# Kernel optimization log

Hardware: AMD Instinct MI355X
Metric: run time of the kernel (lower is better)

## Reference

```python
import jax, jax.numpy as jnp
import numpy as np

B, N, E = 16, 50000, 1600000  # batch, num_nodes (excl. ground), num_edges


def setup_inputs() -> dict:
    key = jax.random.key(0)
    k1, k2, k3, k4 = jax.random.split(key, 4)
    x = jax.random.normal(k1, (B, N), dtype=jnp.float32)
    # node indices in [0, N]; index 0 is the ground node prepended in forward
    src_node = jax.random.randint(k2, (E,), 0, N + 1)
    des_node = jax.random.randint(k3, (E,), 0, N + 1)
    # per-edge device params (a, w, b), gauss init std=0.01 per _init_model_param
    param = jax.random.normal(k4, (3, E), dtype=jnp.float32) * 0.01
    t = jnp.zeros((1,), dtype=jnp.float32)
    return {"t": t, "x": x, "param": param, "src_node": src_node, "des_node": des_node}


def _edge_model(param, v_s, v_d):
    # per-edge nonlinear device current: i_e = a_e * tanh(w_e*(v_s - v_d) + b_e)
    a, w, b = param[0], param[1], param[2]
    return a * jnp.tanh(w * (v_s - v_d) + b)  # (B, E)


def reference(t, x, param, src_node, des_node):
    # prepend ground node (voltage 0) -> aux_v: (B, N+1)
    aux_v = jnp.concatenate([jnp.zeros_like(x[..., :1]), x], axis=-1)
    v_s = aux_v[:, src_node]  # gather (B, E)
    v_d = aux_v[:, des_node]  # gather (B, E)
    state_i = _edge_model(param, v_s, v_d)  # (B, E)
    # KCL: current leaves src, enters des; scatter_add along node axis
    res = jnp.zeros_like(aux_v)
    res = res.at[:, src_node].add(-state_i)
    res = res.at[:, des_node].add(state_i)
    return res[:, 1:]  # drop ground node
```

## Files before the change

### kernel.cpp

```cpp
#include <hip/hip_runtime.h>

#define BATCH 16
#define PS 49
#define NPART 1024
#define SB 256
#define TPB 1024
#define LDSCAP 3840

#define TWO_LOG2E 2.8853900817779268f

__global__ __launch_bounds__(TPB)
void hist1(const int* __restrict__ src, const int* __restrict__ des,
           const float* __restrict__ x, float* __restrict__ auxT,
           unsigned* __restrict__ blockHist, int E, int n) {
    __shared__ unsigned h[NPART];
    __shared__ float tile[64 * 17];
    int tid = threadIdx.x;
    for (int i = tid; i < NPART; i += TPB) h[i] = 0;
    if (blockIdx.x == 0 && tid < BATCH) auxT[tid] = 0.0f;
    int nTiles = (n + 63) / 64;
    for (int t0 = blockIdx.x; t0 < nTiles; t0 += gridDim.x) {
        int i0 = t0 * 64;
        int b = tid >> 6, ii = tid & 63;
        float v = (i0 + ii < n) ? x[(size_t)b * n + i0 + ii] : 0.0f;
        __syncthreads();
        tile[ii * 17 + b] = v;
        __syncthreads();
        int i2 = i0 + (tid >> 4);
        if (i2 < n)
            auxT[(size_t)(i2 + 1) * BATCH + (tid & 15)] = tile[(tid >> 4) * 17 + (tid & 15)];
    }
    __syncthreads();
    long t = (long)blockIdx.x * TPB + tid;
    long stride = (long)gridDim.x * TPB * 4;
    for (long e0 = t * 4; e0 < E; e0 += stride) {
        int ne = (int)min((long)4, (long)E - e0);
        int ss[4], dd[4];
        if (ne == 4) {
            int4 sv = *(const int4*)(src + e0);
            int4 dv = *(const int4*)(des + e0);
            ss[0]=sv.x; ss[1]=sv.y; ss[2]=sv.z; ss[3]=sv.w;
            dd[0]=dv.x; dd[1]=dv.y; dd[2]=dv.z; dd[3]=dv.w;
        } else {
            for (int j = 0; j < ne; ++j) { ss[j] = src[e0+j]; dd[j] = des[e0+j]; }
        }
        for (int j = 0; j < ne; ++j) {
            atomicAdd(&h[ss[j] / PS], 1u);
            atomicAdd(&h[dd[j] / PS], 1u);
        }
    }
    __syncthreads();
    for (int i = tid; i < NPART; i += TPB)
        blockHist[(size_t)blockIdx.x * NPART + i] = h[i];
}

__global__ __launch_bounds__(TPB)
void totals_k(const unsigned* __restrict__ blockHist, unsigned* __restrict__ binTotal) {
    int tid = threadIdx.x;
    int bin = blockIdx.x * 64 + (tid >> 4);
    int j = tid & 15;
    unsigned s = 0;
    for (int r = j; r < SB; r += 16) s += blockHist[(size_t)r * NPART + bin];
#pragma unroll
    for (int m = 1; m < 16; m <<= 1) s += __shfl_xor(s, m, 64);
    if (j == 0) binTotal[bin] = s;
}

__global__ __launch_bounds__(TPB)
void scan_bins(const unsigned* __restrict__ binTotal, unsigned* __restrict__ partStart) {
    __shared__ unsigned wsum[16];
    int tid = threadIdx.x;
    int lane = tid & 63, wv = tid >> 6;
    unsigned v = binTotal[tid];
    unsigned inc = v;
    for (int off = 1; off < 64; off <<= 1) {
        unsigned t = __shfl_up(inc, off, 64);
        if (lane >= off) inc += t;
    }
    if (lane == 63) wsum[wv] = inc;
    __syncthreads();
    if (tid < 16) {
        unsigned w = wsum[tid], winc = w;
        for (int off = 1; off < 16; off <<= 1) {
            unsigned t = __shfl_up(winc, off, 64);
            if (tid >= off) winc += t;
        }
        wsum[tid] = winc - w;
    }
    __syncthreads();
    unsigned excl = (inc - v) + wsum[wv];
    partStart[tid] = excl;
    if (tid == TPB - 1) partStart[NPART] = excl + v;
}

__global__ __launch_bounds__(TPB)
void offs_k(unsigned* __restrict__ blockHist, const unsigned* __restrict__ partStart) {
    int tid = threadIdx.x;
    int binLocal = tid >> 4;
    int bin = blockIdx.x * 64 + binLocal;
    int j = tid & 15;
    const int per = SB / 16;
    unsigned ls = 0;
    for (int r = j * per; r < (j + 1) * per; ++r)
        ls += blockHist[(size_t)r * NPART + bin];
    int waveBase = (binLocal & 3) * 16;
    unsigned excl = 0;
    for (int k = 0; k < 16; ++k) {
        unsigned v = __shfl(ls, waveBase + k, 64);
        if (k < j) excl += v;
    }
    unsigned run = partStart[bin] + excl;
    for (int r = j * per; r < (j + 1) * per; ++r) {
        unsigned tmp = blockHist[(size_t)r * NPART + bin];
        blockHist[(size_t)r * NPART + bin] = run;
        run += tmp;
    }
}

__global__ __launch_bounds__(TPB)
void scatter1(const int* __restrict__ src, const int* __restrict__ des,
              const float* __restrict__ param, const unsigned* __restrict__ offsets,
              uint4* __restrict__ bins, int E) {
    __shared__ unsigned offs[NPART];
    int tid = threadIdx.x;
    for (int i = tid; i < NPART; i += TPB)
        offs[i] = offsets[(size_t)blockIdx.x * NPART + i];
    __syncthreads();
    long t = (long)blockIdx.x * TPB + tid;
    long stride = (long)gridDim.x * TPB * 4;
    for (long e0 = t * 4; e0 < E; e0 += stride) {
        int ne = (int)min((long)4, (long)E - e0);
        int ss[4], dd[4];
        float aa[4], ww[4], cc[4];
        if (ne == 4) {
            int4 sv = *(const int4*)(src + e0);
            int4 dv = *(const int4*)(des + e0);
            float4 av = *(const float4*)(param + e0);
            float4 wv = *(const float4*)(param + E + e0);
            float4 cv = *(const float4*)(param + 2 * (size_t)E + e0);
            ss[0]=sv.x; ss[1]=sv.y; ss[2]=sv.z; ss[3]=sv.w;
            dd[0]=dv.x; dd[1]=dv.y; dd[2]=dv.z; dd[3]=dv.w;
            aa[0]=av.x; aa[1]=av.y; aa[2]=av.z; aa[3]=av.w;
            ww[0]=wv.x; ww[1]=wv.y; ww[2]=wv.z; ww[3]=wv.w;
            cc[0]=cv.x; cc[1]=cv.y; cc[2]=cv.z; cc[3]=cv.w;
        } else {
            for (int j = 0; j < ne; ++j) {
                ss[j] = src[e0+j]; dd[j] = des[e0+j];
                aa[j] = param[e0+j]; ww[j] = param[E + e0 + j];
                cc[j] = param[2 * (size_t)E + e0 + j];
            }
        }
        for (int j = 0; j < ne; ++j) {
            int s = ss[j], d = dd[j];
            float wq = ww[j] * TWO_LOG2E, cq = cc[j] * TWO_LOG2E;
            unsigned slot = atomicAdd(&offs[s / PS], 1u);
            bins[slot] = make_uint4((unsigned)s | ((unsigned)d << 16),
                                    __float_as_uint(-aa[j]), __float_as_uint(wq),
                                    __float_as_uint(cq));
            unsigned slot2 = atomicAdd(&offs[d / PS], 1u);
            bins[slot2] = make_uint4((unsigned)d | ((unsigned)s << 16),
                                     __float_as_uint(aa[j]), __float_as_uint(-wq),
                                     __float_as_uint(cq));
        }
    }
}

static __device__ __forceinline__ float edge_eval(float a, float a2, float wq, float cq,
                                                  float dv) {
    float ez = __builtin_amdgcn_exp2f(__builtin_fmaf(wq, dv, cq));
    float r = __builtin_amdgcn_rcpf(ez + 1.0f);
    return __builtin_fmaf(-a2, r, a);
}

__global__ __launch_bounds__(TPB)
void sort_accumulate(const uint4* __restrict__ bins, const unsigned* __restrict__ partStart,
                     const float* __restrict__ auxT, float* __restrict__ out, int n) {
    extern __shared__ uint4 srec[];
    unsigned* bump = (unsigned*)(srec + LDSCAP);
    unsigned* ns   = bump + PS;
    int p = blockIdx.x;
    int tid = threadIdx.x;
    int lane = tid & 63;
    int wv = tid >> 6;
    unsigned lo = partStart[p], hi = partStart[p + 1];
    unsigned cl = min(hi - lo, (unsigned)LDSCAP);
    int base = p * PS;

    for (int i = tid; i < PS; i += TPB) bump[i] = 0;
    __syncthreads();
    const unsigned* keys = (const unsigned*)bins;
    for (unsigned k = tid; k < cl; k += TPB) {
        unsigned o = keys[(size_t)(lo + k) * 4] & 0xFFFFu;
        atomicAdd(&bump[o - (unsigned)base], 1u);
    }
    __syncthreads();
    if (wv == 0) {
        unsigned v = (lane < PS) ? bump[lane] : 0u;
        unsigned inc = v;
        for (int off = 1; off < 64; off <<= 1) {
            unsigned t = __shfl_up(inc, off, 64);
            if (lane >= off) inc += t;
        }
        unsigned excl = inc - v;
        if (lane < PS) { ns[lane] = excl; bump[lane] = excl; }
        if (lane == PS - 1) ns[PS] = inc;
    }
    __syncthreads();
    for (unsigned k = tid; k < cl; k += TPB) {
        uint4 rec = bins[lo + k];
        unsigned slot = atomicAdd(&bump[(rec.x & 0xFFFFu) - (unsigned)base], 1u);
        srec[slot] = rec;
    }
    __syncthreads();
    int ri = lane >> 2, lj = lane & 3;
    const float4* aux4 = (const float4*)auxT;
    for (int nl = wv; nl < PS; nl += TPB / 64) {
        int node = base + nl;
        if (node == 0 || node > n) continue;
        unsigned l2 = ns[nl], h2 = ns[nl + 1];
        float4 vo = aux4[(size_t)node * 4 + lj];
        float ax = 0.0f, ay = 0.0f, az = 0.0f, as_ = 0.0f;
        for (unsigned kk = l2; kk < h2; kk += 16) {
            unsigned k = kk + (unsigned)ri;
            uint4 rec;
            if (k < h2) rec = srec[k];
            else { rec.x = 0u; rec.y = 0u; rec.z = 0u; rec.w = 0u; }
            unsigned rem = rec.x >> 16;
            float4 vr = aux4[(size_t)rem * 4 + lj];
            float a = __uint_as_float(rec.y);
            float a2 = a + a;
            float wq = __uint_as_float(rec.z);
            float cq = __uint_as_float(rec.w);
            ax  += edge_eval(a, a2, wq, cq, vo.x - vr.x);
            ay  += edge_eval(a, a2, wq, cq, vo.y - vr.y);
            az  += edge_eval(a, a2, wq, cq, vo.z - vr.z);
            as_ += edge_eval(a, a2, wq, cq, vo.w - vr.w);
        }
        for (unsigned kk = lo + cl; kk < hi; kk += 16) {
            unsigned k = kk + (unsigned)ri;
            uint4 rec;
            if (k < hi) rec = bins[k];
            else { rec.x = 0u; rec.y = 0u; rec.z = 0u; rec.w = 0u; }
            if ((int)(rec.x & 0xFFFFu) != node) rec.y = 0u;
            unsigned rem = rec.x >> 16;
            float4 vr = aux4[(size_t)rem * 4 + lj];
            float a = __uint_as_float(rec.y);
            float a2 = a + a;
            float wq = __uint_as_float(rec.z);
            float cq = __uint_as_float(rec.w);
            ax  += edge_eval(a, a2, wq, cq, vo.x - vr.x);
            ay  += edge_eval(a, a2, wq, cq, vo.y - vr.y);
            az  += edge_eval(a, a2, wq, cq, vo.z - vr.z);
            as_ += edge_eval(a, a2, wq, cq, vo.w - vr.w);
        }
#pragma unroll
        for (int m = 4; m < 64; m <<= 1) {
            ax  += __shfl_xor(ax, m, 64);
            ay  += __shfl_xor(ay, m, 64);
            az  += __shfl_xor(az, m, 64);
            as_ += __shfl_xor(as_, m, 64);
        }
        if (lane < 4) {
            int j = node - 1;
            int b0 = lj * 4;
            out[(size_t)(b0 + 0) * n + j] = ax;
            out[(size_t)(b0 + 1) * n + j] = ay;
            out[(size_t)(b0 + 2) * n + j] = az;
            out[(size_t)(b0 + 3) * n + j] = as_;
        }
    }
}

__global__ void edge_direct(const float* __restrict__ param,
                            const int* __restrict__ src,
                            const int* __restrict__ des,
                            const float* __restrict__ x,
                            float* __restrict__ out, int E, int n) {
    int e = blockIdx.x * blockDim.x + threadIdx.x;
    if (e >= E) return;
    float a = param[e], w = param[E + e], c = param[2 * E + e];
    int s = src[e], d = des[e];
#pragma unroll
    for (int b = 0; b < BATCH; ++b) {
        float vs = s ? x[(size_t)b * n + (s - 1)] : 0.0f;
        float vd = d ? x[(size_t)b * n + (d - 1)] : 0.0f;
        float st = a * tanhf(w * (vs - vd) + c);
        if (s) atomicAdd(out + (size_t)b * n + (s - 1), -st);
        if (d) atomicAdd(out + (size_t)b * n + (d - 1), st);
    }
}

extern "C" void kernel_launch(void* const* d_in, const int* in_sizes, int n_in,
                              void* d_out, int out_size, void* d_ws, size_t ws_size,
                              hipStream_t stream) {
    const float* x     = (const float*)d_in[1];
    const float* param = (const float*)d_in[2];
    const int*   src   = (const int*)d_in[3];
    const int*   des   = (const int*)d_in[4];
    float* out = (float*)d_out;

    int E = in_sizes[3];
    int n = in_sizes[1] / BATCH;

    auto alignup = [](size_t v) { return (v + 255) & ~(size_t)255; };
    size_t auxBytes  = alignup((size_t)(n + 1) * BATCH * sizeof(float));
    size_t bhBytes   = alignup((size_t)SB * NPART * sizeof(unsigned));
    size_t psBytes   = alignup((size_t)(NPART + 1) * sizeof(unsigned));
    size_t btBytes   = alignup((size_t)NPART * sizeof(unsigned));
    size_t binBytes  = alignup((size_t)2 * E * sizeof(uint4));
    size_t need      = auxBytes + bhBytes + psBytes + btBytes + binBytes;

    size_t saLds = (size_t)LDSCAP * sizeof(uint4) + (2 * PS + 1 + 8) * sizeof(unsigned);

    if (ws_size >= need && (n + 1) <= NPART * PS && n <= 65534) {
        char* w = (char*)d_ws;
        float*    auxT      = (float*)w;     w += auxBytes;
        unsigned* blockHist = (unsigned*)w;  w += bhBytes;
        unsigned* partStart = (unsigned*)w;  w += psBytes;
        unsigned* binTotal  = (unsigned*)w;  w += btBytes;
        uint4*    bins      = (uint4*)w;

        hist1<<<SB, TPB, 0, stream>>>(src, des, x, auxT, blockHist, E, n);
        totals_k<<<NPART / 64, TPB, 0, stream>>>(blockHist, binTotal);
        scan_bins<<<1, TPB, 0, stream>>>(binTotal, partStart);
        offs_k<<<NPART / 64, TPB, 0, stream>>>(blockHist, partStart);
        scatter1<<<SB, TPB, 0, stream>>>(src, des, param, blockHist, bins, E);
        sort_accumulate<<<NPART, TPB, saLds, stream>>>(bins, partStart, auxT, out, n);
        return;
    }

    (void)hipMemsetAsync(out, 0, (size_t)out_size * sizeof(float), stream);
    edge_direct<<<(E + 255) / 256, 256, 0, stream>>>(param, src, des, x, out, E, n);
}
```

Baseline: 114.0 us.

## Split scatter into two bin-half passes and reuse atomic ranks in local sort

The scatter kernel now makes two passes over the edges, each covering half of the partitions with a half-size shared offset table. The intent is to narrow the write footprint per pass and cut the shared-memory needed per block, at the cost of reading the edge arrays twice. In the per-partition sort, the rank returned by the counting atomic is kept in registers and reused for placement, which removes the second atomic pass. The sort relies on at most four records per thread (4*TPB = 4096 ≥ LDSCAP = 3840).

```diff
diff --git a/kernel.cpp b/kernel.cpp
--- a/kernel.cpp
+++ b/kernel.cpp
@@ -121,46 +121,55 @@
 void scatter1(const int* __restrict__ src, const int* __restrict__ des,
               const float* __restrict__ param, const unsigned* __restrict__ offsets,
               uint4* __restrict__ bins, int E) {
-    __shared__ unsigned offs[NPART];
-    int tid = threadIdx.x;
-    for (int i = tid; i < NPART; i += TPB)
-        offs[i] = offsets[(size_t)blockIdx.x * NPART + i];
-    __syncthreads();
-    long t = (long)blockIdx.x * TPB + tid;
-    long stride = (long)gridDim.x * TPB * 4;
-    for (long e0 = t * 4; e0 < E; e0 += stride) {
-        int ne = (int)min((long)4, (long)E - e0);
-        int ss[4], dd[4];
-        float aa[4], ww[4], cc[4];
-        if (ne == 4) {
-            int4 sv = *(const int4*)(src + e0);
-            int4 dv = *(const int4*)(des + e0);
-            float4 av = *(const float4*)(param + e0);
-            float4 wv = *(const float4*)(param + E + e0);
-            float4 cv = *(const float4*)(param + 2 * (size_t)E + e0);
-            ss[0]=sv.x; ss[1]=sv.y; ss[2]=sv.z; ss[3]=sv.w;
-            dd[0]=dv.x; dd[1]=dv.y; dd[2]=dv.z; dd[3]=dv.w;
-            aa[0]=av.x; aa[1]=av.y; aa[2]=av.z; aa[3]=av.w;
-            ww[0]=wv.x; ww[1]=wv.y; ww[2]=wv.z; ww[3]=wv.w;
-            cc[0]=cv.x; cc[1]=cv.y; cc[2]=cv.z; cc[3]=cv.w;
-        } else {
+    __shared__ unsigned offs[NPART / 2];
+    int tid = threadIdx.x;
+    for (int half = 0; half < 2; ++half) {
+        int binLo = half * (NPART / 2);
+        __syncthreads();
+        for (int i = tid; i < NPART / 2; i += TPB)
+            offs[i] = offsets[(size_t)blockIdx.x * NPART + binLo + i];
+        __syncthreads();
+        long t = (long)blockIdx.x * TPB + tid;
+        long stride = (long)gridDim.x * TPB * 4;
+        for (long e0 = t * 4; e0 < E; e0 += stride) {
+            int ne = (int)min((long)4, (long)E - e0);
+            int ss[4], dd[4];
+            float aa[4], ww[4], cc[4];
+            if (ne == 4) {
+                int4 sv = *(const int4*)(src + e0);
+                int4 dv = *(const int4*)(des + e0);
+                float4 av = *(const float4*)(param + e0);
+                float4 wv = *(const float4*)(param + E + e0);
+                float4 cv = *(const float4*)(param + 2 * (size_t)E + e0);
+                ss[0]=sv.x; ss[1]=sv.y; ss[2]=sv.z; ss[3]=sv.w;
+                dd[0]=dv.x; dd[1]=dv.y; dd[2]=dv.z; dd[3]=dv.w;
+                aa[0]=av.x; aa[1]=av.y; aa[2]=av.z; aa[3]=av.w;
+                ww[0]=wv.x; ww[1]=wv.y; ww[2]=wv.z; ww[3]=wv.w;
+                cc[0]=cv.x; cc[1]=cv.y; cc[2]=cv.z; cc[3]=cv.w;
+            } else {
+                for (int j = 0; j < ne; ++j) {
+                    ss[j] = src[e0+j]; dd[j] = des[e0+j];
+                    aa[j] = param[e0+j]; ww[j] = param[E + e0 + j];
+                    cc[j] = param[2 * (size_t)E + e0 + j];
+                }
+            }
             for (int j = 0; j < ne; ++j) {
-                ss[j] = src[e0+j]; dd[j] = des[e0+j];
-                aa[j] = param[e0+j]; ww[j] = param[E + e0 + j];
-                cc[j] = param[2 * (size_t)E + e0 + j];
+                int s = ss[j], d = dd[j];
+                float wq = ww[j] * TWO_LOG2E, cq = cc[j] * TWO_LOG2E;
+                int ps = s / PS, pd = d / PS;
+                if ((ps >> 9) == half) {
+                    unsigned slot = atomicAdd(&offs[ps & 511], 1u);
+                    bins[slot] = make_uint4((unsigned)s | ((unsigned)d << 16),
+                                            __float_as_uint(-aa[j]), __float_as_uint(wq),
+                                            __float_as_uint(cq));
+                }
+                if ((pd >> 9) == half) {
+                    unsigned slot2 = atomicAdd(&offs[pd & 511], 1u);
+                    bins[slot2] = make_uint4((unsigned)d | ((unsigned)s << 16),
+                                             __float_as_uint(aa[j]), __float_as_uint(-wq),
+                                             __float_as_uint(cq));
+                }
             }
-        }
-        for (int j = 0; j < ne; ++j) {
-            int s = ss[j], d = dd[j];
-            float wq = ww[j] * TWO_LOG2E, cq = cc[j] * TWO_LOG2E;
-            unsigned slot = atomicAdd(&offs[s / PS], 1u);
-            bins[slot] = make_uint4((unsigned)s | ((unsigned)d << 16),
-                                    __float_as_uint(-aa[j]), __float_as_uint(wq),
-                                    __float_as_uint(cq));
-            unsigned slot2 = atomicAdd(&offs[d / PS], 1u);
-            bins[slot2] = make_uint4((unsigned)d | ((unsigned)s << 16),
-                                     __float_as_uint(aa[j]), __float_as_uint(-wq),
-                                     __float_as_uint(cq));
         }
     }
 }
@@ -189,10 +198,17 @@
     for (int i = tid; i < PS; i += TPB) bump[i] = 0;
     __syncthreads();
     const unsigned* keys = (const unsigned*)bins;
-    for (unsigned k = tid; k < cl; k += TPB) {
-        unsigned o = keys[(size_t)(lo + k) * 4] & 0xFFFFu;
-        atomicAdd(&bump[o - (unsigned)base], 1u);
-    }
+    unsigned o0 = 0, o1 = 0, o2 = 0, o3 = 0;
+    unsigned rk0 = 0, rk1 = 0, rk2 = 0, rk3 = 0;
+    unsigned k0 = tid, k1 = tid + TPB, k2 = tid + 2 * TPB, k3 = tid + 3 * TPB;
+    if (k0 < cl) { o0 = (keys[(size_t)(lo + k0) * 4] & 0xFFFFu) - (unsigned)base;
+                   rk0 = atomicAdd(&bump[o0], 1u); }
+    if (k1 < cl) { o1 = (keys[(size_t)(lo + k1) * 4] & 0xFFFFu) - (unsigned)base;
+                   rk1 = atomicAdd(&bump[o1], 1u); }
+    if (k2 < cl) { o2 = (keys[(size_t)(lo + k2) * 4] & 0xFFFFu) - (unsigned)base;
+                   rk2 = atomicAdd(&bump[o2], 1u); }
+    if (k3 < cl) { o3 = (keys[(size_t)(lo + k3) * 4] & 0xFFFFu) - (unsigned)base;
+                   rk3 = atomicAdd(&bump[o3], 1u); }
     __syncthreads();
     if (wv == 0) {
         unsigned v = (lane < PS) ? bump[lane] : 0u;
@@ -201,16 +217,14 @@
             unsigned t = __shfl_up(inc, off, 64);
             if (lane >= off) inc += t;
         }
-        unsigned excl = inc - v;
-        if (lane < PS) { ns[lane] = excl; bump[lane] = excl; }
+        if (lane < PS) ns[lane] = inc - v;
         if (lane == PS - 1) ns[PS] = inc;
     }
     __syncthreads();
-    for (unsigned k = tid; k < cl; k += TPB) {
-        uint4 rec = bins[lo + k];
-        unsigned slot = atomicAdd(&bump[(rec.x & 0xFFFFu) - (unsigned)base], 1u);
-        srec[slot] = rec;
-    }
+    if (k0 < cl) srec[ns[o0] + rk0] = bins[lo + k0];
+    if (k1 < cl) srec[ns[o1] + rk1] = bins[lo + k1];
+    if (k2 < cl) srec[ns[o2] + rk2] = bins[lo + k2];
+    if (k3 < cl) srec[ns[o3] + rk3] = bins[lo + k3];
     __syncthreads();
     int ri = lane >> 2, lj = lane & 3;
     const float4* aux4 = (const float4*)auxT;
```

New measurement: 108.8 us (median of 2 runs). -4.6%, faster.
